# Kernel tuning notes

Measured on AMD Instinct MI355X. Metric: run time of the kernel, lower is better.

The kernel has to match this reference:

```python
import jax, jax.numpy as jnp
import numpy as np
from jax import lax

EPS = 1e-5
KH, KW, PAD, DIL = 3, 3, 1, 1


def _bilinear_gather(x, py, px):
    """x: [B,C,H,W]; py/px: [B,K,H,W] float sample coords. Returns [B,C,K,H,W].
    Zero-padding semantics (torchvision deform_conv2d): corners outside the image contribute 0."""
    B, C, H, W = x.shape
    K = py.shape[1]
    y0 = jnp.floor(py)
    x0 = jnp.floor(px)
    wy1 = py - y0
    wy0 = 1.0 - wy1
    wx1 = px - x0
    wx0 = 1.0 - wx1
    xf = x.reshape(B, C, H * W)

    def corner(yc, xc, w):
        valid = (yc >= 0) & (yc <= H - 1) & (xc >= 0) & (xc <= W - 1)
        yi = jnp.clip(yc, 0, H - 1).astype(jnp.int32)
        xi = jnp.clip(xc, 0, W - 1).astype(jnp.int32)
        lin = (yi * W + xi).reshape(B, -1)  # [B, K*H*W]
        v = jax.vmap(lambda xb, lb: xb[:, lb])(xf, lin)  # [B, C, K*H*W]
        return v * (w * valid.astype(x.dtype)).reshape(B, 1, -1)

    out = (corner(y0, x0, wy0 * wx0)
           + corner(y0, x0 + 1.0, wy0 * wx1)
           + corner(y0 + 1.0, x0, wy1 * wx0)
           + corner(y0 + 1.0, x0 + 1.0, wy1 * wx1))
    return out.reshape(B, C, K, H, W)


def _deform_conv(x, offset, w):
    B, C, H, W = x.shape
    K = KH * KW
    off = offset.reshape(B, K, 2, H, W)  # (dy, dx) per kernel tap
    ki = (jnp.arange(K) // KW - PAD).astype(x.dtype)  # kernel row offset (dil=1)
    kj = (jnp.arange(K) % KW - PAD).astype(x.dtype)
    hh = jnp.arange(H).astype(x.dtype)
    ww = jnp.arange(W).astype(x.dtype)
    py = hh[None, None, :, None] + ki[None, :, None, None] + off[:, :, 0]
    px = ww[None, None, None, :] + kj[None, :, None, None] + off[:, :, 1]
    val = _bilinear_gather(x, py, px)  # [B,C,K,H,W]
    return jnp.einsum('bckhw,ock->bohw', val, w.reshape(w.shape[0], C, K))


def _bn(x, gamma, beta, mean, var):
    inv = gamma * lax.rsqrt(var + EPS)
    return x * inv[None, :, None, None] + (beta - mean * inv)[None, :, None, None]


def setup_inputs() -> dict:
    key = jax.random.key(0)
    ks = jax.random.split(key, 12)
    B, C, H, W = 4, 128, 128, 128
    return {
        'x': jax.random.normal(ks[0], (B, C, H, W), jnp.float32),
        'offset': jax.random.normal(ks[1], (B, 2 * KH * KW, H, W), jnp.float32),
        'w1': jax.random.normal(ks[2], (C, C, KH, KW), jnp.float32) * 0.05,
        'bn1_gamma': jax.random.uniform(ks[3], (C,), jnp.float32, 0.5, 1.5),
        'bn1_beta': jax.random.normal(ks[4], (C,), jnp.float32) * 0.1,
        'bn1_mean': jax.random.normal(ks[5], (C,), jnp.float32) * 0.1,
        'bn1_var': jax.random.uniform(ks[6], (C,), jnp.float32, 0.5, 1.5),
        'w2': jax.random.normal(ks[7], (C, C, KH, KW), jnp.float32) * 0.05,
        'bn2_gamma': jax.random.uniform(ks[8], (C,), jnp.float32, 0.5, 1.5),
        'bn2_beta': jax.random.normal(ks[9], (C,), jnp.float32) * 0.1,
        'bn2_mean': jax.random.normal(ks[10], (C,), jnp.float32) * 0.1,
        'bn2_var': jax.random.uniform(ks[11], (C,), jnp.float32, 0.5, 1.5),
    }


def reference(x, offset, w1, bn1_gamma, bn1_beta, bn1_mean, bn1_var,
              w2, bn2_gamma, bn2_beta, bn2_mean, bn2_var):
    identity = x
    out = _deform_conv(x, offset, w1)
    out = jax.nn.relu(_bn(out, bn1_gamma, bn1_beta, bn1_mean, bn1_var))
    out = lax.conv_general_dilated(out, w2, window_strides=(1, 1),
                                   padding=((PAD, PAD), (PAD, PAD)),
                                   dimension_numbers=('NCHW', 'OIHW', 'NCHW'))
    out = _bn(out, bn2_gamma, bn2_beta, bn2_mean, bn2_var)
    out = jax.nn.relu(out + identity)
    return out
```

## Files before the change

### kernel.cpp

```cpp
#include <hip/hip_runtime.h>
#include <hip/hip_fp16.h>
#include <stdint.h>

#define B_ 4
#define C_ 128
#define H_ 128
#define W_ 128
#define HW 16384

typedef _Float16 h8 __attribute__((ext_vector_type(8)));
typedef float f32x16 __attribute__((ext_vector_type(16)));

__device__ __forceinline__ unsigned cvtpk_f16(float lo, float hi) {
    auto r = __builtin_amdgcn_cvt_pkrtz(lo, hi);
    return *(unsigned*)&r;
}

__device__ __forceinline__ unsigned blend_h2(unsigned c0, unsigned c1, unsigned c2, unsigned c3,
                                             __half2 G0, __half2 G1, __half2 G2, __half2 G3) {
    __half2 s = __hmul2(G0, *(__half2*)&c0);
    s = __hfma2(G1, *(__half2*)&c1, s);
    s = __hfma2(G2, *(__half2*)&c2, s);
    s = __hfma2(G3, *(__half2*)&c3, s);
    return *(unsigned*)&s;
}

__device__ __forceinline__ void gll16(const void* g, void* l) {
    __builtin_amdgcn_global_load_lds((const unsigned int*)g, (unsigned int*)l, 16, 0, 0);
}

#define PBAR() do { \
    asm volatile("s_waitcnt lgkmcnt(0)" ::: "memory"); \
    __builtin_amdgcn_s_barrier(); \
    asm volatile("" ::: "memory"); \
} while (0)
#define CBAR() do { \
    asm volatile("" ::: "memory"); \
    __builtin_amdgcn_s_barrier(); \
    asm volatile("" ::: "memory"); \
} while (0)

__global__ __launch_bounds__(256) void prep_all(const float* __restrict__ x,
                                                unsigned short* __restrict__ xh,
                                                const float* __restrict__ w1,
                                                const float* __restrict__ w2,
                                                unsigned short* __restrict__ w1f,
                                                unsigned short* __restrict__ w2f,
                                                unsigned short* __restrict__ o1p,
                                                const float* g1, const float* b1, const float* m1, const float* v1,
                                                const float* g2, const float* b2, const float* m2, const float* v2,
                                                float* inv1, float* sh1, float* inv2, float* sh2) {
    __shared__ unsigned short tile[32][36];
    int blk = blockIdx.x;
    int tid = threadIdx.x;
    if (blk >= 1282) {
        int nb = blk - 1282;
        int wt = nb & 3, ct = (nb >> 2) & 3, h = (nb >> 4) & 127, b = nb >> 11;
        int c = tid >> 3, seg = tid & 7;
        const float* srcp = x + ((size_t)((b * 128 + ct * 32 + c) * 128 + h) * 128) + wt * 32 + seg * 4;
        float4 v = *(const float4*)srcp;
        uint2 pk;
        pk.x = cvtpk_f16(v.x, v.y);
        pk.y = cvtpk_f16(v.z, v.w);
        *(uint2*)&tile[c][seg * 4] = pk;
        __syncthreads();
        int w = tid >> 3, s2 = tid & 7;
        unsigned a0 = tile[s2 * 4 + 0][w];
        unsigned a1 = tile[s2 * 4 + 1][w];
        unsigned a2 = tile[s2 * 4 + 2][w];
        unsigned a3 = tile[s2 * 4 + 3][w];
        uint2 o;
        o.x = (a1 << 16) | a0;
        o.y = (a3 << 16) | a2;
        *(uint2*)(xh + ((size_t)((b * 128 + h) * 128 + wt * 32 + w) * 128) + ct * 32 + s2 * 4) = o;
        return;
    }
    if (blk < 1152) {
        int i = blk * 256 + tid;
        const float* src = w1;
        unsigned short* dst = w1f;
        int j = i;
        if (i >= 147456) { j = i - 147456; src = w2; dst = w2f; }
        int o = j / 1152, rem = j % 1152;
        int c = rem / 9, tap = rem % 9;
        _Float16 hv = (_Float16)src[j];
        int s = o >> 5;
        int ks = c >> 4;
        int l = (o & 31) | (((c >> 3) & 1) << 5);
        int jj = c & 7;
        dst[(((tap * 4 + s) * 8 + ks) * 64 + l) * 8 + jj] = *(unsigned short*)&hv;
    } else if (blk < 1281) {
        int i = (blk - 1152) * 256 + tid;
        if (i < 33024) {
            int chunk = i & 15;
            int pos = i >> 4;
            int b = pos / 516;
            int r = pos % 516;
            int row, col;
            if (r < 130)      { row = 0;   col = r; }
            else if (r < 260) { row = 129; col = r - 130; }
            else { int j = r - 260; row = 1 + (j >> 1); col = (j & 1) * 129; }
            uint4 z = {0u, 0u, 0u, 0u};
            *(uint4*)((char*)o1p + (size_t)((b * 130 + row) * 130 + col) * 256 + chunk * 16) = z;
        }
    } else {
        if (tid < 128) {
            float iv = g1[tid] * rsqrtf(v1[tid] + 1e-5f);
            inv1[tid] = iv; sh1[tid] = b1[tid] - m1[tid] * iv;
        } else {
            int u = tid - 128;
            float iv = g2[u] * rsqrtf(v2[u] + 1e-5f);
            inv2[u] = iv; sh2[u] = b2[u] - m2[u] * iv;
        }
    }
}

__global__ __launch_bounds__(512, 4) void gemm1_k(
    const unsigned short* __restrict__ xh,
    const float* __restrict__ off,
    const unsigned short* __restrict__ w1f,
    const float* __restrict__ inv1,
    const float* __restrict__ sh1,
    unsigned short* __restrict__ out1p) {
    __shared__ __align__(16) char ldsv[2][16384];

    int bid = blockIdx.x;
    int swz = ((bid & 7) << 7) | (bid >> 3);
    int half = swz & 1, h = (swz >> 1) & 127, b = swz >> 8;
    int w0 = half * 64;
    int tid = threadIdx.x;
    int bH = b * H_;
    const char* xb8 = (const char*)xh;

    if (tid < 256) {
        int prow = tid >> 4;
        int seg = tid & 15;
        int sb = seg * 16;

        float dy[2][4], dx[2][4];
        float g[2][4][4];
        unsigned PX[4][4];
        uint4 buf[4][4];

#define OFFLOAD(TT) do { \
    int dyB_ = ((b * 18 + 2 * (TT)) * H_ + h) * W_ + w0; \
    _Pragma("unroll") \
    for (int c_ = 0; c_ < 4; ++c_) { \
        int p_ = prow + c_ * 16; \
        dy[(TT) & 1][c_] = off[dyB_ + p_]; \
        dx[(TT) & 1][c_] = off[dyB_ + HW + p_]; \
    } \
} while (0)

#define COORD(TT) do { \
    int kh_ = (TT) / 3 - 1, kw_ = (TT) % 3 - 1; \
    _Pragma("unroll") \
    for (int c_ = 0; c_ < 4; ++c_) { \
        int p_ = prow + c_ * 16; \
        float py_ = (float)(h + kh_) + dy[(TT) & 1][c_]; \
        float px_ = (float)(w0 + p_ + kw_) + dx[(TT) & 1][c_]; \
        float y0f_ = floorf(py_), x0f_ = floorf(px_); \
        int y0_ = (int)y0f_, x0_ = (int)x0f_; \
        float wy1_ = py_ - y0f_, wx1_ = px_ - x0f_; \
        float wy0_ = 1.f - wy1_, wx0_ = 1.f - wx1_; \
        int y1_ = y0_ + 1, x1_ = x0_ + 1; \
        g[(TT) & 1][c_][0] = ((unsigned)y0_ < 128u && (unsigned)x0_ < 128u) ? wy0_ * wx0_ : 0.f; \
        g[(TT) & 1][c_][1] = ((unsigned)y0_ < 128u && (unsigned)x1_ < 128u) ? wy0_ * wx1_ : 0.f; \
        g[(TT) & 1][c_][2] = ((unsigned)y1_ < 128u && (unsigned)x0_ < 128u) ? wy1_ * wx0_ : 0.f; \
        g[(TT) & 1][c_][3] = ((unsigned)y1_ < 128u && (unsigned)x1_ < 128u) ? wy1_ * wx1_ : 0.f; \
        int y0c_ = min(max(y0_, 0), 127), y1c_ = min(max(y1_, 0), 127); \
        int x0c_ = min(max(x0_, 0), 127), x1c_ = min(max(x1_, 0), 127); \
        int r0_ = (bH + y0c_) * W_, r1_ = (bH + y1c_) * W_; \
        PX[c_][0] = (unsigned)((r0_ + x0c_) * 256) + sb; \
        PX[c_][1] = (unsigned)((r0_ + x1c_) * 256) + sb; \
        PX[c_][2] = (unsigned)((r1_ + x0c_) * 256) + sb; \
        PX[c_][3] = (unsigned)((r1_ + x1c_) * 256) + sb; \
    } \
} while (0)

#define ISSUE_ALL() do { \
    _Pragma("unroll") \
    for (int c_ = 0; c_ < 4; ++c_) \
        _Pragma("unroll") \
        for (int k_ = 0; k_ < 4; ++k_) buf[c_][k_] = *(const uint4*)(xb8 + PX[c_][k_]); \
} while (0)

#define BLEND_ALL(TT) do { \
    char* vdst_ = &ldsv[(TT) & 1][0]; \
    _Pragma("unroll") \
    for (int c_ = 0; c_ < 4; ++c_) { \
        __half2 G0_ = __float2half2_rn(g[(TT) & 1][c_][0]); \
        __half2 G1_ = __float2half2_rn(g[(TT) & 1][c_][1]); \
        __half2 G2_ = __float2half2_rn(g[(TT) & 1][c_][2]); \
        __half2 G3_ = __float2half2_rn(g[(TT) & 1][c_][3]); \
        uint4 st_; \
        st_.x = blend_h2(buf[c_][0].x, buf[c_][1].x, buf[c_][2].x, buf[c_][3].x, G0_, G1_, G2_, G3_); \
        st_.y = blend_h2(buf[c_][0].y, buf[c_][1].y, buf[c_][2].y, buf[c_][3].y, G0_, G1_, G2_, G3_); \
        st_.z = blend_h2(buf[c_][0].z, buf[c_][1].z, buf[c_][2].z, buf[c_][3].z, G0_, G1_, G2_, G3_); \
        st_.w = blend_h2(buf[c_][0].w, buf[c_][1].w, buf[c_][2].w, buf[c_][3].w, G0_, G1_, G2_, G3_); \
        int row_ = prow + c_ * 16; \
        *(uint4*)(vdst_ + row_ * 256 + ((seg ^ (row_ & 15)) << 4)) = st_; \
    } \
} while (0)

        OFFLOAD(0);
        COORD(0);
        ISSUE_ALL();
        OFFLOAD(1);
        BLEND_ALL(0);
        COORD(1);
        ISSUE_ALL();
        OFFLOAD(2);
        PBAR();

        #pragma unroll
        for (int t = 0; t < 9; ++t) {
            if (t < 8) BLEND_ALL(t + 1);
            if (t < 7) { COORD(t + 2); ISSUE_ALL(); }
            if (t + 3 <= 8) OFFLOAD(t + 3);
            PBAR();
        }
#undef OFFLOAD
#undef COORD
#undef ISSUE_ALL
#undef BLEND_ALL
    } else {
        int ctid = tid - 256;
        int lane = ctid & 63, wq = ctid >> 6;
        int lp = lane & 31, hi = lane >> 5;
        int lsw = lp & 15;
        int bRow0 = lp * 256;
        int bRow1 = (32 + lp) * 256;

        f32x16 acc0 = {};
        f32x16 acc1 = {};
        h8 wreg[2][8];

        {
            const unsigned short* wb = w1f + wq * 4096 + lane * 8;
            #pragma unroll
            for (int ks = 0; ks < 8; ++ks) wreg[0][ks] = *(const h8*)(wb + ks * 512);
        }
        CBAR();
        #pragma unroll
        for (int t = 0; t < 9; ++t) {
            if (t < 8) {
                const unsigned short* wb = w1f + ((t + 1) * 4 + wq) * 4096 + lane * 8;
                #pragma unroll
                for (int ks = 0; ks < 8; ++ks) wreg[(t + 1) & 1][ks] = *(const h8*)(wb + ks * 512);
            }
            const char* vcur = &ldsv[t & 1][0];
            #pragma unroll
            for (int ks = 0; ks < 8; ++ks) {
                int q0 = 2 * ks + hi;
                int sl = (q0 ^ lsw) << 4;
                h8 b0 = *(const h8*)(vcur + bRow0 + sl);
                h8 b1 = *(const h8*)(vcur + bRow1 + sl);
                h8 a = wreg[t & 1][ks];
                acc0 = __builtin_amdgcn_mfma_f32_32x32x16_f16(a, b0, acc0, 0, 0, 0);
                acc1 = __builtin_amdgcn_mfma_f32_32x32x16_f16(a, b1, acc1, 0, 0, 0);
            }
            CBAR();
        }

        #pragma unroll
        for (int j = 0; j < 2; ++j) {
            int p = w0 + j * 32 + lp;
            size_t rowbase = (size_t)((b * 130 + h + 1) * 130 + 1 + p) * 128;
            #pragma unroll
            for (int k = 0; k < 4; ++k) {
                int o0 = wq * 32 + k * 8 + hi * 4;
                float4 iv = *(const float4*)(inv1 + o0);
                float4 sv = *(const float4*)(sh1 + o0);
                float e0, e1, e2, e3;
                if (j == 0) {
                    e0 = acc0[4 * k + 0]; e1 = acc0[4 * k + 1];
                    e2 = acc0[4 * k + 2]; e3 = acc0[4 * k + 3];
                } else {
                    e0 = acc1[4 * k + 0]; e1 = acc1[4 * k + 1];
                    e2 = acc1[4 * k + 2]; e3 = acc1[4 * k + 3];
                }
                float v0 = fmaxf(fmaf(e0, iv.x, sv.x), 0.f);
                float v1 = fmaxf(fmaf(e1, iv.y, sv.y), 0.f);
                float v2 = fmaxf(fmaf(e2, iv.z, sv.z), 0.f);
                float v3 = fmaxf(fmaf(e3, iv.w, sv.w), 0.f);
                uint2 pk2;
                pk2.x = cvtpk_f16(v0, v1);
                pk2.y = cvtpk_f16(v2, v3);
                *(uint2*)(out1p + rowbase + o0) = pk2;
            }
        }
    }
}

__global__ __launch_bounds__(512, 4) void gemm2_k(
    const unsigned short* __restrict__ out1p,
    const unsigned short* __restrict__ w2f,
    const unsigned short* __restrict__ xh,
    const float* __restrict__ inv2,
    const float* __restrict__ sh2,
    float* __restrict__ outp) {
    __shared__ __align__(16) char ldsS[33280];

    int bid = blockIdx.x;
    int swz = ((bid & 7) << 6) | (bid >> 3);
    int h = swz & 127, b = swz >> 7;
    int tid = threadIdx.x, lane = tid & 63, wv = tid >> 6;
    int wq = wv >> 1, wp = wv & 1;
    int lp = lane & 31, hi = lane >> 5;
    int lsw = lp & 15;

    f32x16 acc0 = {};
    f32x16 acc1 = {};
    h8 wreg[2][8];

    {
        const unsigned short* wb = w2f + wq * 4096 + lane * 8;
        #pragma unroll
        for (int ks = 0; ks < 8; ++ks) wreg[0][ks] = *(const h8*)(wb + ks * 512);
    }

    #pragma unroll
    for (int t = 0; t < 9; ++t) {
        int kh = t / 3, kw = t % 3;
        if (kw == 0) {
            __syncthreads();
            const char* srow = (const char*)out1p + (size_t)((b * 130 + h + kh) * 130) * 256;
            #pragma unroll
            for (int it = 0; it < 5; ++it) {
                int ci = it * 512 + tid;
                if (ci < 2080) {
                    int r = ci >> 4, q = ci & 15;
                    gll16(srow + r * 256 + ((q ^ (r & 15)) << 4), ldsS + ci * 16);
                }
            }
            __syncthreads();
        }
        if (t < 8) {
            const unsigned short* wb = w2f + ((t + 1) * 4 + wq) * 4096 + lane * 8;
            #pragma unroll
            for (int ks = 0; ks < 8; ++ks) wreg[(t + 1) & 1][ks] = *(const h8*)(wb + ks * 512);
        }
        #pragma unroll
        for (int ks = 0; ks < 8; ++ks) {
            int q0 = 2 * ks + hi;
            int pr0 = wp * 64 + lp + kw;
            int pr1 = pr0 + 32;
            h8 b0 = *(const h8*)(ldsS + pr0 * 256 + ((q0 ^ (pr0 & 15)) << 4));
            h8 b1 = *(const h8*)(ldsS + pr1 * 256 + ((q0 ^ (pr1 & 15)) << 4));
            h8 a = wreg[t & 1][ks];
            acc0 = __builtin_amdgcn_mfma_f32_32x32x16_f16(a, b0, acc0, 0, 0, 0);
            acc1 = __builtin_amdgcn_mfma_f32_32x32x16_f16(a, b1, acc1, 0, 0, 0);
        }
    }

    #pragma unroll
    for (int j = 0; j < 2; ++j) {
        int p = wp * 64 + j * 32 + lp;
        const unsigned short* xrow = xh + (size_t)((b * 128 + h) * 128 + p) * 128;
        #pragma unroll
        for (int k = 0; k < 4; ++k) {
            int o0 = wq * 32 + k * 8 + hi * 4;
            uint2 rx = *(const uint2*)(xrow + o0);
            __half2 hx0 = *(__half2*)&rx.x;
            __half2 hx1 = *(__half2*)&rx.y;
            float x0 = __low2float(hx0), x1 = __high2float(hx0);
            float x2 = __low2float(hx1), x3 = __high2float(hx1);
            float e0, e1, e2, e3;
            if (j == 0) {
                e0 = acc0[4 * k + 0]; e1 = acc0[4 * k + 1];
                e2 = acc0[4 * k + 2]; e3 = acc0[4 * k + 3];
            } else {
                e0 = acc1[4 * k + 0]; e1 = acc1[4 * k + 1];
                e2 = acc1[4 * k + 2]; e3 = acc1[4 * k + 3];
            }
            size_t idx = ((size_t)(b * C_ + o0) * H_ + h) * W_ + p;
            outp[idx]            = fmaxf(fmaf(e0, inv2[o0 + 0], sh2[o0 + 0]) + x0, 0.f);
            outp[idx + HW]       = fmaxf(fmaf(e1, inv2[o0 + 1], sh2[o0 + 1]) + x1, 0.f);
            outp[idx + 2 * HW]   = fmaxf(fmaf(e2, inv2[o0 + 2], sh2[o0 + 2]) + x2, 0.f);
            outp[idx + 3 * HW]   = fmaxf(fmaf(e3, inv2[o0 + 3], sh2[o0 + 3]) + x3, 0.f);
        }
    }
}

extern "C" void kernel_launch(void* const* d_in, const int* in_sizes, int n_in,
                              void* d_out, int out_size, void* d_ws, size_t ws_size,
                              hipStream_t stream) {
    const float* x   = (const float*)d_in[0];
    const float* off = (const float*)d_in[1];
    const float* w1  = (const float*)d_in[2];
    const float* g1  = (const float*)d_in[3];
    const float* b1  = (const float*)d_in[4];
    const float* m1  = (const float*)d_in[5];
    const float* v1  = (const float*)d_in[6];
    const float* w2  = (const float*)d_in[7];
    const float* g2  = (const float*)d_in[8];
    const float* b2  = (const float*)d_in[9];
    const float* m2  = (const float*)d_in[10];
    const float* v2  = (const float*)d_in[11];
    float* outp = (float*)d_out;

    char* ws = (char*)d_ws;
    unsigned short* w1f = (unsigned short*)(ws);
    unsigned short* w2f = (unsigned short*)(ws + 294912);
    float* inv1 = (float*)(ws + 589824);
    float* sh1  = (float*)(ws + 590336);
    float* inv2 = (float*)(ws + 590848);
    float* sh2  = (float*)(ws + 591360);
    unsigned short* xh  = (unsigned short*)(ws + 591872);
    unsigned short* o1p = (unsigned short*)(ws + 17369088);

    prep_all<<<9474, 256, 0, stream>>>(x, xh, w1, w2, w1f, w2f, o1p,
                                       g1, b1, m1, v1, g2, b2, m2, v2,
                                       inv1, sh1, inv2, sh2);
    gemm1_k<<<1024, 512, 0, stream>>>(xh, off, w1f, inv1, sh1, o1p);
    gemm2_k<<<512, 512, 0, stream>>>(o1p, w2f, xh, inv2, sh2, outp);
}
```

Measured before the change: 84.18 us.

## Stage GEMM1 epilogue through LDS and prefetch GEMM2 input rows into registers

```diff
diff --git a/kernel.cpp b/kernel.cpp
--- a/kernel.cpp
+++ b/kernel.cpp
@@ -224,6 +224,7 @@
 #undef COORD
 #undef ISSUE_ALL
 #undef BLEND_ALL
+        CBAR();
     } else {
         int ctid = tid - 256;
         int lane = ctid & 63, wq = ctid >> 6;
@@ -263,10 +264,10 @@
             CBAR();
         }
 
+        char* eb = &ldsv[0][0];
         #pragma unroll
         for (int j = 0; j < 2; ++j) {
-            int p = w0 + j * 32 + lp;
-            size_t rowbase = (size_t)((b * 130 + h + 1) * 130 + 1 + p) * 128;
+            int row = j * 32 + lp;
             #pragma unroll
             for (int k = 0; k < 4; ++k) {
                 int o0 = wq * 32 + k * 8 + hi * 4;
@@ -287,8 +288,22 @@
                 uint2 pk2;
                 pk2.x = cvtpk_f16(v0, v1);
                 pk2.y = cvtpk_f16(v2, v3);
-                *(uint2*)(out1p + rowbase + o0) = pk2;
-            }
+                int q = wq * 4 + k;
+                *(uint2*)(eb + row * 256 + ((q ^ (row & 15)) << 4) + hi * 8) = pk2;
+            }
+        }
+        PBAR();
+    }
+
+    {
+        const char* eb = &ldsv[0][0];
+        char* dstg = (char*)out1p + ((size_t)((b * 130 + h + 1) * 130 + 1 + w0)) * 256;
+        #pragma unroll
+        for (int it = 0; it < 2; ++it) {
+            int ci = it * 512 + tid;
+            int row = ci >> 4, q = ci & 15;
+            uint4 v = *(const uint4*)(eb + row * 256 + ((q ^ (row & 15)) << 4));
+            *(uint4*)(dstg + ci * 16) = v;
         }
     }
 }
@@ -308,33 +323,41 @@
     int tid = threadIdx.x, lane = tid & 63, wv = tid >> 6;
     int wq = wv >> 1, wp = wv & 1;
     int lp = lane & 31, hi = lane >> 5;
-    int lsw = lp & 15;
 
     f32x16 acc0 = {};
     f32x16 acc1 = {};
     h8 wreg[2][8];
+    uint4 stg[4];
+    uint4 stg4;
 
     {
         const unsigned short* wb = w2f + wq * 4096 + lane * 8;
         #pragma unroll
         for (int ks = 0; ks < 8; ++ks) wreg[0][ks] = *(const h8*)(wb + ks * 512);
+    }
+
+    {
+        const char* srow = (const char*)out1p + (size_t)((b * 130 + h) * 130) * 256;
+        #pragma unroll
+        for (int it = 0; it < 5; ++it) {
+            int ci = it * 512 + tid;
+            if (ci < 2080) {
+                int r = ci >> 4, q = ci & 15;
+                gll16(srow + r * 256 + ((q ^ (r & 15)) << 4), ldsS + ci * 16);
+            }
+        }
+        __syncthreads();
     }
 
     #pragma unroll
     for (int t = 0; t < 9; ++t) {
         int kh = t / 3, kw = t % 3;
-        if (kw == 0) {
-            __syncthreads();
-            const char* srow = (const char*)out1p + (size_t)((b * 130 + h + kh) * 130) * 256;
-            #pragma unroll
-            for (int it = 0; it < 5; ++it) {
-                int ci = it * 512 + tid;
-                if (ci < 2080) {
-                    int r = ci >> 4, q = ci & 15;
-                    gll16(srow + r * 256 + ((q ^ (r & 15)) << 4), ldsS + ci * 16);
-                }
-            }
-            __syncthreads();
+        if (kw == 1 && kh < 2) {
+            const char* srow = (const char*)out1p + (size_t)((b * 130 + h + kh + 1) * 130) * 256;
+            #pragma unroll
+            for (int it = 0; it < 4; ++it)
+                stg[it] = *(const uint4*)(srow + (it * 512 + tid) * 16);
+            if (tid < 32) stg4 = *(const uint4*)(srow + (2048 + tid) * 16);
         }
         if (t < 8) {
             const unsigned short* wb = w2f + ((t + 1) * 4 + wq) * 4096 + lane * 8;
@@ -351,6 +374,23 @@
             h8 a = wreg[t & 1][ks];
             acc0 = __builtin_amdgcn_mfma_f32_32x32x16_f16(a, b0, acc0, 0, 0, 0);
             acc1 = __builtin_amdgcn_mfma_f32_32x32x16_f16(a, b1, acc1, 0, 0, 0);
+        }
+        if (kw == 2 && kh < 2) {
+            __syncthreads();
+            asm volatile("s_waitcnt vmcnt(0)" ::: "memory");
+            #pragma unroll
+            for (int it = 0; it < 4; ++it) {
+                int ci = it * 512 + tid;
+                int r = ci >> 4, q = ci & 15;
+                *(uint4*)(ldsS + r * 256 + (((q) ^ (r & 15)) << 4)) = stg[it];
+            }
+            if (tid < 32) {
+                int ci = 2048 + tid;
+                int r = ci >> 4, q = ci & 15;
+                *(uint4*)(ldsS + r * 256 + (((q) ^ (r & 15)) << 4)) = stg4;
+            }
+            asm volatile("s_waitcnt lgkmcnt(0)" ::: "memory");
+            __syncthreads();
         }
     }
 
```

New measurement: 92.70 us. 10.1% more time.
